# Kernel optimization log

Hardware: AMD Instinct MI355X
Metric: run time of the kernel (lower is better)

## Reference

```python
import jax, jax.numpy as jnp
import numpy as np

B, N, C, H, W = 256, 50000, 3, 32, 32


def setup_inputs() -> dict:
    key = jax.random.key(0)
    k1, k2, k3 = jax.random.split(key, 3)
    inp = jax.random.normal(k1, (B, C, H, W), dtype=jnp.float32)
    train_data = jax.random.normal(k2, (N, C, H, W), dtype=jnp.float32)
    # per-query noise levels in a realistic diffusion range
    sigma = jax.random.uniform(k3, (B,), dtype=jnp.float32) * 1.5 + 0.5
    return {"input": inp, "sigma": sigma, "train_data": train_data}


def reference(input, sigma, train_data):
    """Karras optimal denoiser:
    D(x, sigma) = sum_i y_i * Gau(x; y_i, sigma^2 I) / sum_i Gau(x; y_i, sigma^2 I).
    The Gaussian normalization constant (sigma*sqrt(2*pi))^D cancels in the ratio,
    so this is exactly softmax over -0.5*||x - y_i||^2 / sigma^2 (same math as the
    per-dim product of densities in the original, computed stably in log space).
    """
    b = input.shape[0]
    x = input.reshape(b, -1)                      # [B, D]
    y = train_data.reshape(train_data.shape[0], -1)  # [N, D]
    x2 = jnp.sum(x * x, axis=1, keepdims=True)    # [B, 1]
    y2 = jnp.sum(y * y, axis=1)                   # [N]
    # pairwise squared distances via GEMM: [B, N]
    sqdist = x2 + y2[None, :] - 2.0 * (x @ y.T)
    logw = -0.5 * sqdist / (sigma[:, None] ** 2)  # [B, N]
    w = jax.nn.softmax(logw, axis=1)              # normalized Gaussian weights
    out = w @ y                                   # [B, D] weighted average
    return out.reshape(input.shape)
```

## Files before the change

kernel.cpp:

```cpp
#include <hip/hip_runtime.h>
#include <hip/hip_bf16.h>
#include <type_traits>

#define BQ   256
#define NTR  50000
#define DD   3072
#define NSP  50048
#define NBLK 782
#define CAP  4096
#define DELTA 18.0f

typedef __fp16 f16;
typedef __fp16 f16x2 __attribute__((ext_vector_type(2)));
typedef __fp16 f16x8 __attribute__((ext_vector_type(8)));
typedef float  f32x4 __attribute__((ext_vector_type(4)));

__global__ __launch_bounds__(256) void kx(const float* __restrict__ x, f16* __restrict__ xp) {
    const int t = blockIdx.x * 256 + threadIdx.x;
    const int g = t >> 8, r = t & 255;
    const f32x4* src = (const f32x4*)(x + (size_t)r * DD + (g << 3));
    f32x4 a = src[0], b = src[1];
    union { f16x2 h2[4]; f16x8 h8; } u;
    u.h2[0] = __builtin_amdgcn_cvt_pkrtz(a[0], a[1]);
    u.h2[1] = __builtin_amdgcn_cvt_pkrtz(a[2], a[3]);
    u.h2[2] = __builtin_amdgcn_cvt_pkrtz(b[0], b[1]);
    u.h2[3] = __builtin_amdgcn_cvt_pkrtz(b[2], b[3]);
    ((f16x8*)xp)[t] = u.h8;
}

__global__ __launch_bounds__(256, 2) void kqk(
    const f16* __restrict__ xp, const float* __restrict__ y,
    float* __restrict__ S, float* __restrict__ pmax) {
    __shared__ char Bs[2][8192];

    const int tid = threadIdx.x;
    const int blk = blockIdx.x;
    const int n0  = blk * 64;

    const int ry   = tid >> 2;
    const int kp   = (tid & 3) << 4;
    const int yrow = n0 + ry;
    const bool yval = yrow < NTR;
    const float* ybase = y + (size_t)yrow * DD + kp;
    const int bsw = (ry & 7) << 4;
    const int bo0 = ry * 128 + (((kp << 1) +  0) ^ bsw);
    const int bo1 = ry * 128 + (((kp << 1) + 16) ^ bsw);

    const int w = tid >> 6, l = tid & 63;
    const int l15 = l & 15, lg = l >> 4;

    f32x4 acc[4][4] = {};
    float y2a = 0.f;
    f32x4 p0, p1, p2, p3, q0, q1, q2, q3;

    auto loady = [&](f32x4& a0, f32x4& a1, f32x4& a2, f32x4& a3, int ks) {
        if (yval) {
            const f32x4* p = (const f32x4*)(ybase + (ks << 6));
            a0 = p[0]; a1 = p[1]; a2 = p[2]; a3 = p[3];
        } else { a0 = 0.f; a1 = 0.f; a2 = 0.f; a3 = 0.f; }
    };
    auto cvtw = [&](f32x4& a0, f32x4& a1, f32x4& a2, f32x4& a3, int buf) {
        y2a += a0[0]*a0[0] + a0[1]*a0[1] + a0[2]*a0[2] + a0[3]*a0[3]
             + a1[0]*a1[0] + a1[1]*a1[1] + a1[2]*a1[2] + a1[3]*a1[3]
             + a2[0]*a2[0] + a2[1]*a2[1] + a2[2]*a2[2] + a2[3]*a2[3]
             + a3[0]*a3[0] + a3[1]*a3[1] + a3[2]*a3[2] + a3[3]*a3[3];
        union { f16x2 h2[4]; f16x8 h8; } u0, u1;
        u0.h2[0] = __builtin_amdgcn_cvt_pkrtz(a0[0], a0[1]);
        u0.h2[1] = __builtin_amdgcn_cvt_pkrtz(a0[2], a0[3]);
        u0.h2[2] = __builtin_amdgcn_cvt_pkrtz(a1[0], a1[1]);
        u0.h2[3] = __builtin_amdgcn_cvt_pkrtz(a1[2], a1[3]);
        u1.h2[0] = __builtin_amdgcn_cvt_pkrtz(a2[0], a2[1]);
        u1.h2[1] = __builtin_amdgcn_cvt_pkrtz(a2[2], a2[3]);
        u1.h2[2] = __builtin_amdgcn_cvt_pkrtz(a3[0], a3[1]);
        u1.h2[3] = __builtin_amdgcn_cvt_pkrtz(a3[2], a3[3]);
        *(f16x8*)(&Bs[buf][bo0]) = u0.h8;
        *(f16x8*)(&Bs[buf][bo1]) = u1.h8;
    };

    loady(p0, p1, p2, p3, 0);
    loady(q0, q1, q2, q3, 1);
    cvtw(p0, p1, p2, p3, 0);
    asm volatile("s_waitcnt lgkmcnt(0)" ::: "memory");
    __builtin_amdgcn_s_barrier();

    const f16x8* ap = (const f16x8*)xp;
    const int arow = (w << 6) + l15;

    auto iter = [&](int ks, auto curC,
                    f32x4& s0, f32x4& s1, f32x4& s2, f32x4& s3,
                    f32x4& t0, f32x4& t1, f32x4& t2, f32x4& t3) {
        constexpr int cur = decltype(curC)::value;
        f16x8 af[2][4];
        #pragma unroll
        for (int kk = 0; kk < 2; ++kk)
            #pragma unroll
            for (int fm = 0; fm < 4; ++fm)
                af[kk][fm] = ap[(size_t)((ks << 3) + (kk << 2) + lg) * 256 + arow + (fm << 4)];
        if (ks + 2 < 48) loady(s0, s1, s2, s3, ks + 2);
        f16x8 bf[2][4];
        #pragma unroll
        for (int kk = 0; kk < 2; ++kk)
            #pragma unroll
            for (int fn = 0; fn < 4; ++fn) {
                int r = (fn << 4) + l15;
                bf[kk][fn] = *(const f16x8*)(&Bs[cur][r * 128 + (((kk << 6) + (lg << 4)) ^ ((r & 7) << 4))]);
            }
        #pragma unroll
        for (int kk = 0; kk < 2; ++kk)
            #pragma unroll
            for (int fm = 0; fm < 4; ++fm)
                #pragma unroll
                for (int fn = 0; fn < 4; ++fn)
                    acc[fm][fn] = __builtin_amdgcn_mfma_f32_16x16x32_f16(af[kk][fm], bf[kk][fn], acc[fm][fn], 0, 0, 0);
        if (ks + 1 < 48) cvtw(t0, t1, t2, t3, cur ^ 1);
        asm volatile("s_waitcnt lgkmcnt(0)" ::: "memory");
        __builtin_amdgcn_s_barrier();
    };

    for (int ks2 = 0; ks2 < 48; ks2 += 2) {
        iter(ks2,     std::integral_constant<int,0>{}, p0,p1,p2,p3, q0,q1,q2,q3);
        iter(ks2 + 1, std::integral_constant<int,1>{}, q0,q1,q2,q3, p0,p1,p2,p3);
    }

    float* lys = (float*)&Bs[0][0];
    y2a += __shfl_xor(y2a, 1, 64);
    y2a += __shfl_xor(y2a, 2, 64);
    if ((tid & 3) == 0) lys[ry] = y2a;
    __syncthreads();
    float ly2[4];
    #pragma unroll
    for (int fn = 0; fn < 4; ++fn) ly2[fn] = 0.5f * lys[(fn << 4) + l15];
    #pragma unroll
    for (int fm = 0; fm < 4; ++fm) {
        #pragma unroll
        for (int j = 0; j < 4; ++j) {
            float rm = -3.4e38f;
            #pragma unroll
            for (int fn = 0; fn < 4; ++fn) {
                int col = n0 + (fn << 4) + l15;
                float sc = acc[fm][fn][j] - ly2[fn];
                rm = (col < NTR) ? fmaxf(rm, sc) : rm;
            }
            #pragma unroll
            for (int off = 1; off < 16; off <<= 1) rm = fmaxf(rm, __shfl_xor(rm, off, 64));
            if (l15 == 0)
                pmax[(size_t)((w << 6) + (fm << 4) + (lg << 2) + j) * NBLK + blk] = rm;
        }
    }
    #pragma unroll
    for (int fm = 0; fm < 4; ++fm) {
        int row0 = (w << 6) + (fm << 4) + (lg << 2);
        #pragma unroll
        for (int fn = 0; fn < 4; ++fn) {
            int col = n0 + (fn << 4) + l15;
            float* sp = S + (size_t)row0 * NSP + col;
            sp[0]               = acc[fm][fn][0] - ly2[fn];
            sp[NSP]             = acc[fm][fn][1] - ly2[fn];
            sp[2 * (size_t)NSP] = acc[fm][fn][2] - ly2[fn];
            sp[3 * (size_t)NSP] = acc[fm][fn][3] - ly2[fn];
        }
    }
}

__global__ __launch_bounds__(256) void ksel(
    const float* __restrict__ S, const float* __restrict__ pmax,
    const float* __restrict__ sig, unsigned* __restrict__ cnt,
    unsigned* __restrict__ cand) {
    __shared__ float red[4];
    const int b = blockIdx.x, tid = threadIdx.x;
    const float s2 = sig[b] * sig[b];
    const float* pm = pmax + (size_t)b * NBLK;
    float mx = -3.4e38f;
    for (int i = tid; i < NBLK; i += 256) mx = fmaxf(mx, pm[i]);
    #pragma unroll
    for (int o = 1; o < 64; o <<= 1) mx = fmaxf(mx, __shfl_xor(mx, o, 64));
    if ((tid & 63) == 0) red[tid >> 6] = mx;
    __syncthreads();
    mx = fmaxf(fmaxf(red[0], red[1]), fmaxf(red[2], red[3]));
    const float thr = mx - DELTA * s2;
    const f32x4* rowv = (const f32x4*)(S + (size_t)b * NSP);
    for (int i = tid; i < 12500; i += 256) {
        f32x4 s = rowv[i];
        #pragma unroll
        for (int j = 0; j < 4; ++j) {
            if (s[j] >= thr) {
                unsigned idx = atomicAdd(&cnt[b], 1u);
                if (idx < CAP) cand[(size_t)b * CAP + idx] = (unsigned)(4 * i + j);
            }
        }
    }
}

__global__ __launch_bounds__(512) void kpv(
    const float* __restrict__ x, const float* __restrict__ y,
    const float* __restrict__ sig, const unsigned* __restrict__ cnt,
    const unsigned* __restrict__ cand, float* __restrict__ out) {
    __shared__ float xs[DD];
    __shared__ unsigned ci[CAP];
    __shared__ float om[8], ol[8];
    __shared__ float sumv[DD];
    const int b = blockIdx.x, tid = threadIdx.x;
    const int c = (int)(cnt[b] < (unsigned)CAP ? cnt[b] : (unsigned)CAP);
    const float s2 = sig[b] * sig[b];
    const float isc = -0.5f / s2;
    for (int i = tid; i < DD; i += 512) xs[i] = x[(size_t)b * DD + i];
    for (int i = tid; i < c; i += 512) ci[i] = cand[(size_t)b * CAP + i];
    __syncthreads();
    const int w = tid >> 6, l = tid & 63;
    const f32x4* xr = (const f32x4*)xs;

    f32x4 o[12] = {};
    float m = -3.4e38f, ll = 0.f;
    f32x4 A[12], Bv[12];

    auto LD = [&](f32x4* dst, int i) {
        const f32x4* yr = (const f32x4*)(y + (size_t)ci[i] * DD);
        #pragma unroll
        for (int j = 0; j < 12; ++j) dst[j] = yr[(j << 6) + l];
    };
    auto PROC = [&](f32x4* src) {
        float d2 = 0.f;
        #pragma unroll
        for (int j = 0; j < 12; ++j) {
            f32x4 xv = xr[(j << 6) + l];
            float a0 = xv[0]-src[j][0], a1 = xv[1]-src[j][1],
                  a2 = xv[2]-src[j][2], a3 = xv[3]-src[j][3];
            d2 += a0*a0 + a1*a1 + a2*a2 + a3*a3;
        }
        #pragma unroll
        for (int off = 1; off < 64; off <<= 1) d2 += __shfl_xor(d2, off, 64);
        float s = d2 * isc;
        float mn = fmaxf(m, s);
        float f = __expf(m - mn);
        float wi = __expf(s - mn);
        #pragma unroll
        for (int j = 0; j < 12; ++j) o[j] = o[j] * f + wi * src[j];
        ll = ll * f + wi;
        m = mn;
    };

    int i = w;
    if (i < c) LD(A, i);
    for (; i < c; i += 16) {
        int i2 = i + 8;
        if (i2 < c) LD(Bv, i2);
        PROC(A);
        if (i2 < c) {
            if (i + 16 < c) LD(A, i + 16);
            PROC(Bv);
        }
    }
    om[w] = m; ol[w] = ll;
    __syncthreads();
    float M = om[0];
    #pragma unroll
    for (int ww = 1; ww < 8; ++ww) M = fmaxf(M, om[ww]);
    float Ls = 0.f;
    #pragma unroll
    for (int ww = 0; ww < 8; ++ww) Ls += ol[ww] * __expf(om[ww] - M);
    const float fw = __expf(m - M);
    f32x4* sv = (f32x4*)sumv;
    if (w == 0) {
        #pragma unroll
        for (int j = 0; j < 12; ++j) sv[(j << 6) + l] = o[j] * fw;
    }
    __syncthreads();
    for (int ww = 1; ww < 8; ++ww) {
        if (w == ww) {
            #pragma unroll
            for (int j = 0; j < 12; ++j) sv[(j << 6) + l] += o[j] * fw;
        }
        __syncthreads();
    }
    const float inv = 1.f / Ls;
    f32x4* od = (f32x4*)(out + (size_t)b * DD);
    for (int t = tid; t < 768; t += 512) od[t] = sv[t] * inv;
}

extern "C" void kernel_launch(void* const* d_in, const int* in_sizes, int n_in,
                              void* d_out, int out_size, void* d_ws, size_t ws_size,
                              hipStream_t stream) {
    const float* x   = (const float*)d_in[0];
    const float* sig = (const float*)d_in[1];
    const float* y   = (const float*)d_in[2];
    float* out = (float*)d_out;
    char* ws = (char*)d_ws;
    f16*      xp   = (f16*)(ws);
    unsigned* cnt  = (unsigned*)(ws + 1572864);
    unsigned* cand = (unsigned*)(ws + 1573888);
    float*    pmax = (float*)(ws + 5768192);
    float*    S    = (float*)(ws + 6568960);

    (void)hipMemsetAsync(cnt, 0, 256 * sizeof(unsigned), stream);
    kx  <<<384, 256, 0, stream>>>(x, xp);
    kqk <<<NBLK, 256, 0, stream>>>(xp, y, S, pmax);
    ksel<<<256, 256, 0, stream>>>(S, pmax, sig, cnt, cand);
    kpv <<<256, 512, 0, stream>>>(x, y, sig, cnt, cand, out);
}
```

Measured before the change: 291.1 us.

## Widen QK tile to 128 train rows per block and single-stage prefetch

Each block of the distance GEMM now covers 128 training rows instead of 64, so there are half as many blocks, and each loaded A fragment from the query matrix feeds twice as many MFMAs. The double-register y prefetch (two stages ahead) becomes a single-stage prefetch of 8 vectors per thread, and the accumulator grows to 4x8 tiles. The goal is to reduce redundant A-operand global loads and per-block overhead. The cost is higher register pressure under launch_bounds(256,2), a shallower prefetch that hides less load latency, and fewer blocks for the GPU's CUs.

```diff
diff --git a/kernel.cpp b/kernel.cpp
--- a/kernel.cpp
+++ b/kernel.cpp
@@ -6,7 +6,7 @@
 #define NTR  50000
 #define DD   3072
 #define NSP  50048
-#define NBLK 782
+#define NBLK 391
 #define CAP  4096
 #define DELTA 18.0f
 
@@ -31,112 +31,107 @@
 __global__ __launch_bounds__(256, 2) void kqk(
     const f16* __restrict__ xp, const float* __restrict__ y,
     float* __restrict__ S, float* __restrict__ pmax) {
-    __shared__ char Bs[2][8192];
+    __shared__ char Bs[2][16384];
 
     const int tid = threadIdx.x;
     const int blk = blockIdx.x;
-    const int n0  = blk * 64;
-
-    const int ry   = tid >> 2;
-    const int kp   = (tid & 3) << 4;
+    const int n0  = blk * 128;
+
+    const int ry   = tid >> 1;
+    const int kp   = (tid & 1) << 5;
     const int yrow = n0 + ry;
     const bool yval = yrow < NTR;
     const float* ybase = y + (size_t)yrow * DD + kp;
     const int bsw = (ry & 7) << 4;
-    const int bo0 = ry * 128 + (((kp << 1) +  0) ^ bsw);
-    const int bo1 = ry * 128 + (((kp << 1) + 16) ^ bsw);
+    int bo[4];
+    #pragma unroll
+    for (int j = 0; j < 4; ++j) bo[j] = ry * 128 + (((kp << 1) + (j << 4)) ^ bsw);
 
     const int w = tid >> 6, l = tid & 63;
     const int l15 = l & 15, lg = l >> 4;
 
-    f32x4 acc[4][4] = {};
+    f32x4 acc[4][8] = {};
     float y2a = 0.f;
-    f32x4 p0, p1, p2, p3, q0, q1, q2, q3;
-
-    auto loady = [&](f32x4& a0, f32x4& a1, f32x4& a2, f32x4& a3, int ks) {
+    f32x4 p[8];
+
+    auto loady = [&](int ks) {
         if (yval) {
-            const f32x4* p = (const f32x4*)(ybase + (ks << 6));
-            a0 = p[0]; a1 = p[1]; a2 = p[2]; a3 = p[3];
-        } else { a0 = 0.f; a1 = 0.f; a2 = 0.f; a3 = 0.f; }
-    };
-    auto cvtw = [&](f32x4& a0, f32x4& a1, f32x4& a2, f32x4& a3, int buf) {
-        y2a += a0[0]*a0[0] + a0[1]*a0[1] + a0[2]*a0[2] + a0[3]*a0[3]
-             + a1[0]*a1[0] + a1[1]*a1[1] + a1[2]*a1[2] + a1[3]*a1[3]
-             + a2[0]*a2[0] + a2[1]*a2[1] + a2[2]*a2[2] + a2[3]*a2[3]
-             + a3[0]*a3[0] + a3[1]*a3[1] + a3[2]*a3[2] + a3[3]*a3[3];
-        union { f16x2 h2[4]; f16x8 h8; } u0, u1;
-        u0.h2[0] = __builtin_amdgcn_cvt_pkrtz(a0[0], a0[1]);
-        u0.h2[1] = __builtin_amdgcn_cvt_pkrtz(a0[2], a0[3]);
-        u0.h2[2] = __builtin_amdgcn_cvt_pkrtz(a1[0], a1[1]);
-        u0.h2[3] = __builtin_amdgcn_cvt_pkrtz(a1[2], a1[3]);
-        u1.h2[0] = __builtin_amdgcn_cvt_pkrtz(a2[0], a2[1]);
-        u1.h2[1] = __builtin_amdgcn_cvt_pkrtz(a2[2], a2[3]);
-        u1.h2[2] = __builtin_amdgcn_cvt_pkrtz(a3[0], a3[1]);
-        u1.h2[3] = __builtin_amdgcn_cvt_pkrtz(a3[2], a3[3]);
-        *(f16x8*)(&Bs[buf][bo0]) = u0.h8;
-        *(f16x8*)(&Bs[buf][bo1]) = u1.h8;
-    };
-
-    loady(p0, p1, p2, p3, 0);
-    loady(q0, q1, q2, q3, 1);
-    cvtw(p0, p1, p2, p3, 0);
+            const f32x4* pp = (const f32x4*)(ybase + (ks << 6));
+            #pragma unroll
+            for (int j = 0; j < 8; ++j) p[j] = pp[j];
+        } else {
+            #pragma unroll
+            for (int j = 0; j < 8; ++j) p[j] = 0.f;
+        }
+    };
+    auto cvtw = [&](int buf) {
+        #pragma unroll
+        for (int j = 0; j < 8; ++j)
+            y2a += p[j][0]*p[j][0] + p[j][1]*p[j][1] + p[j][2]*p[j][2] + p[j][3]*p[j][3];
+        union { f16x2 h2[4]; f16x8 h8; } u[4];
+        #pragma unroll
+        for (int j = 0; j < 4; ++j) {
+            u[j].h2[0] = __builtin_amdgcn_cvt_pkrtz(p[2*j][0],   p[2*j][1]);
+            u[j].h2[1] = __builtin_amdgcn_cvt_pkrtz(p[2*j][2],   p[2*j][3]);
+            u[j].h2[2] = __builtin_amdgcn_cvt_pkrtz(p[2*j+1][0], p[2*j+1][1]);
+            u[j].h2[3] = __builtin_amdgcn_cvt_pkrtz(p[2*j+1][2], p[2*j+1][3]);
+            *(f16x8*)(&Bs[buf][bo[j]]) = u[j].h8;
+        }
+    };
+
+    loady(0);
+    cvtw(0);
     asm volatile("s_waitcnt lgkmcnt(0)" ::: "memory");
     __builtin_amdgcn_s_barrier();
 
     const f16x8* ap = (const f16x8*)xp;
     const int arow = (w << 6) + l15;
 
-    auto iter = [&](int ks, auto curC,
-                    f32x4& s0, f32x4& s1, f32x4& s2, f32x4& s3,
-                    f32x4& t0, f32x4& t1, f32x4& t2, f32x4& t3) {
-        constexpr int cur = decltype(curC)::value;
-        f16x8 af[2][4];
-        #pragma unroll
-        for (int kk = 0; kk < 2; ++kk)
+    for (int ks = 0; ks < 48; ++ks) {
+        const int cur = ks & 1;
+        if (ks + 1 < 48) loady(ks + 1);
+        #pragma unroll
+        for (int kk = 0; kk < 2; ++kk) {
+            f16x8 af[4];
             #pragma unroll
             for (int fm = 0; fm < 4; ++fm)
-                af[kk][fm] = ap[(size_t)((ks << 3) + (kk << 2) + lg) * 256 + arow + (fm << 4)];
-        if (ks + 2 < 48) loady(s0, s1, s2, s3, ks + 2);
-        f16x8 bf[2][4];
-        #pragma unroll
-        for (int kk = 0; kk < 2; ++kk)
-            #pragma unroll
-            for (int fn = 0; fn < 4; ++fn) {
-                int r = (fn << 4) + l15;
-                bf[kk][fn] = *(const f16x8*)(&Bs[cur][r * 128 + (((kk << 6) + (lg << 4)) ^ ((r & 7) << 4))]);
+                af[fm] = ap[(size_t)((ks << 3) + (kk << 2) + lg) * 256 + arow + (fm << 4)];
+            #pragma unroll
+            for (int fnh = 0; fnh < 2; ++fnh) {
+                f16x8 bf[4];
+                #pragma unroll
+                for (int fj = 0; fj < 4; ++fj) {
+                    int fn = (fnh << 2) + fj;
+                    int r = (fn << 4) + l15;
+                    bf[fj] = *(const f16x8*)(&Bs[cur][r * 128 + (((kk << 6) + (lg << 4)) ^ ((r & 7) << 4))]);
+                }
+                #pragma unroll
+                for (int fm = 0; fm < 4; ++fm)
+                    #pragma unroll
+                    for (int fj = 0; fj < 4; ++fj)
+                        acc[fm][(fnh << 2) + fj] =
+                            __builtin_amdgcn_mfma_f32_16x16x32_f16(af[fm], bf[fj], acc[fm][(fnh << 2) + fj], 0, 0, 0);
             }
-        #pragma unroll
-        for (int kk = 0; kk < 2; ++kk)
-            #pragma unroll
-            for (int fm = 0; fm < 4; ++fm)
-                #pragma unroll
-                for (int fn = 0; fn < 4; ++fn)
-                    acc[fm][fn] = __builtin_amdgcn_mfma_f32_16x16x32_f16(af[kk][fm], bf[kk][fn], acc[fm][fn], 0, 0, 0);
-        if (ks + 1 < 48) cvtw(t0, t1, t2, t3, cur ^ 1);
+        }
+        if (ks + 1 < 48) cvtw(cur ^ 1);
         asm volatile("s_waitcnt lgkmcnt(0)" ::: "memory");
         __builtin_amdgcn_s_barrier();
-    };
-
-    for (int ks2 = 0; ks2 < 48; ks2 += 2) {
-        iter(ks2,     std::integral_constant<int,0>{}, p0,p1,p2,p3, q0,q1,q2,q3);
-        iter(ks2 + 1, std::integral_constant<int,1>{}, q0,q1,q2,q3, p0,p1,p2,p3);
     }
 
     float* lys = (float*)&Bs[0][0];
     y2a += __shfl_xor(y2a, 1, 64);
-    y2a += __shfl_xor(y2a, 2, 64);
-    if ((tid & 3) == 0) lys[ry] = y2a;
-    __syncthreads();
-    float ly2[4];
-    #pragma unroll
-    for (int fn = 0; fn < 4; ++fn) ly2[fn] = 0.5f * lys[(fn << 4) + l15];
+    if ((tid & 1) == 0) lys[ry] = y2a;
+    __syncthreads();
+    float ly2[8];
+    #pragma unroll
+    for (int fn = 0; fn < 8; ++fn) ly2[fn] = 0.5f * lys[(fn << 4) + l15];
     #pragma unroll
     for (int fm = 0; fm < 4; ++fm) {
         #pragma unroll
         for (int j = 0; j < 4; ++j) {
             float rm = -3.4e38f;
             #pragma unroll
-            for (int fn = 0; fn < 4; ++fn) {
+            for (int fn = 0; fn < 8; ++fn) {
                 int col = n0 + (fn << 4) + l15;
                 float sc = acc[fm][fn][j] - ly2[fn];
                 rm = (col < NTR) ? fmaxf(rm, sc) : rm;
@@ -151,7 +146,7 @@
     for (int fm = 0; fm < 4; ++fm) {
         int row0 = (w << 6) + (fm << 4) + (lg << 2);
         #pragma unroll
-        for (int fn = 0; fn < 4; ++fn) {
+        for (int fn = 0; fn < 8; ++fn) {
             int col = n0 + (fn << 4) + l15;
             float* sp = S + (size_t)row0 * NSP + col;
             sp[0]               = acc[fm][fn][0] - ly2[fn];
```

After: 303.3 us. +4.2%, slower.
